# Optimization experiments

Hardware: AMD Instinct MI355X
Metric: run time of the kernel (lower is better)

## Reference

```python
import jax, jax.numpy as jnp
import numpy as np

B, N, EMB, FEAT = 4, 32, 512, 512
DO = N * (N - 1) // 2  # do_num = 0.5*N*(N-1)


def _encoder(h, adj, Wt, a_src, a_dst):
    # GATencoderlayer (inferred): single-head GAT attention restricted to the
    # strictly-lower triangle so that I_A = I - attn is unit lower-triangular
    # (invertible) and causal_graph = I - I_A = attn is a nonneg. strict-lower DAG.
    feat = h @ Wt  # [B,N,F]
    scores = jax.nn.leaky_relu((feat @ a_src)[:, :, None] + (feat @ a_dst)[:, None, :], 0.2)
    strict_lower = jnp.tril(jnp.ones((N, N), dtype=bool), -1)
    mask = (adj > 0) & strict_lower
    attn = jax.nn.softmax(jnp.where(mask, scores, -1e9), axis=-1)
    attn = jnp.where(mask.any(-1, keepdims=True), attn, 0.0) * mask  # row 0 has no parents
    fU = jax.nn.relu(attn @ feat)  # [B,N,F]
    I_A = jnp.eye(N, dtype=h.dtype) - attn
    return fU, I_A[:, None]  # I_A: [B,1,N,N] (multihead=1)


def _decoder(h, W, Wt):
    # GATdecoderlayer (inferred): aggregate linearly-transformed features with the
    # provided (sampled) mixing matrix W.
    feat = h @ Wt  # [B',N,F]
    return jax.nn.relu(jnp.einsum('bij,bjf->bif', W[:, 0], feat))


def _computing(cg, eps_do, few, feb, fsw, fsb):
    # Vectorized form of the triple-nested do-calculus loops.
    # cg: [B,N,N] strictly-lower causal graph.
    Bc = cg.shape[0]
    a, b = np.triu_indices(N, 1)  # raw_do pairs, same (i<j) row-major order as the loops
    idx = np.arange(N)
    ja = idx[None, :] == a[:, None]  # [DO,N]
    jb = idx[None, :] == b[:, None]
    lower = np.tril(np.ones((N, N), dtype=bool), -1)  # j < i (loop range j<=i, i==j handled by eye)
    pos = cg > 0  # [B,N,N]
    P = (pos & jnp.asarray(lower)).astype(cg.dtype)  # parent sets pa(i) = {k<i: cg[i,k]>0}
    common = jnp.einsum('bik,bjk->bij', P, P) > 0    # pa(i) \cap pa(j) nonempty
    ja_ = ja[:, None, :]; jb_ = jb[:, None, :]       # j-axis one-hots [DO,1,N]
    ia_ = ja[:, :, None]; ib_ = jb[:, :, None]       # i-axis one-hots [DO,N,1]
    c23 = jnp.asarray(lower[None] & ((ja_ & ~ib_) | (jb_ & ~ia_)))          # [DO,N,N]
    c4 = jnp.asarray(lower[None] & ~ja_ & ~jb_ & ~ia_ & ~ib_)               # [DO,N,N]
    eye = jnp.eye(N, dtype=bool)
    label = eye[None, None] | (c23[None] & pos[:, None]) | (c4[None] & common[:, None])  # [B,DO,N,N]
    # intervened graph: zero rows a and b
    keep = jnp.asarray(~(ja | jb)).astype(cg.dtype)  # [DO,N]
    cgd = (cg[:, None] * keep[None, :, :, None]).reshape(Bc * DO, N, N) + jnp.eye(N, dtype=cg.dtype)
    I_A = jnp.linalg.inv(cgd)[:, None]  # [B*DO,1,N,N]
    e = few[0, 0] * I_A + feb[0]  # Linear(1,1) applied elementwise
    s = fsw[0, 0] * I_A + fsb[0]
    z = e + jnp.exp(0.5 * s) * eps_do  # VAE reparameterization
    W_do = jnp.where(I_A == 0, I_A, z)
    return label.reshape(Bc * DO, N, N).astype(cg.dtype), W_do


def _forward(doc_sents_h, adj, enc_Wt, enc_asrc, enc_adst, dec_Wt, fce_w, fce_b, fcs_w, fcs_b, eps_main, eps_do):
    fU, I_A = _encoder(doc_sents_h, adj, enc_Wt, enc_asrc, enc_adst)
    causal_graph = jnp.eye(N, dtype=doc_sents_h.dtype) - I_A  # [B,1,N,N]
    inv = jnp.linalg.inv(I_A)
    e = fce_w[0, 0] * inv + fce_b[0]
    s = fcs_w[0, 0] * inv + fcs_b[0]
    z = e + jnp.exp(0.5 * s) * eps_main
    W = jnp.where(inv == 0, inv, z)
    X_raw = _decoder(fU, W, dec_Wt)
    label, W_do = _computing(causal_graph[:, 0], eps_do, fce_w, fce_b, fcs_w, fcs_b)
    h_do = jnp.broadcast_to(fU[:, None], (B, DO, N, FEAT)).reshape(B * DO, N, FEAT)
    X_do = _decoder(h_do, W_do, dec_Wt)
    return X_raw, X_do, label, causal_graph, e, s


def setup_inputs():
    key = jax.random.key(0)
    ks = jax.random.split(key, 10)
    return {
        'doc_sents_h': jax.random.normal(ks[0], (B, N, EMB), jnp.float32) * 0.5,
        'adj': jnp.ones((B, N, N), jnp.float32),
        'doc_len': jnp.full((B,), N, jnp.int32),
        'enc_Wt': jax.random.normal(ks[1], (EMB, FEAT), jnp.float32) / np.sqrt(EMB).astype(np.float32),
        'enc_asrc': jax.random.normal(ks[2], (FEAT,), jnp.float32) * 0.1,
        'enc_adst': jax.random.normal(ks[3], (FEAT,), jnp.float32) * 0.1,
        'dec_Wt': jax.random.normal(ks[4], (FEAT, FEAT), jnp.float32) / np.sqrt(FEAT).astype(np.float32),
        'fce_w': jax.random.normal(ks[5], (1, 1), jnp.float32) * 0.1,
        'fce_b': jax.random.normal(ks[6], (1,), jnp.float32) * 0.1,
        'fcs_w': jax.random.normal(ks[7], (1, 1), jnp.float32) * 0.1,
        'fcs_b': jax.random.normal(ks[8], (1,), jnp.float32) * 0.1,
        'eps_main': jax.random.normal(ks[9], (B, 1, N, N), jnp.float32),
        'eps_do': jax.random.normal(jax.random.fold_in(key, 1), (B * DO, 1, N, N), jnp.float32),
    }


def reference(doc_sents_h, adj, doc_len, enc_Wt, enc_asrc, enc_adst, dec_Wt, fce_w, fce_b, fcs_w, fcs_b, eps_main, eps_do):
    del doc_len  # original only asserts max(doc_len) == max_doc_len
    return _forward(doc_sents_h, adj, enc_Wt, enc_asrc, enc_adst, dec_Wt, fce_w, fce_b, fcs_w, fcs_b, eps_main, eps_do)
```

## Files before the change

kernel.cpp:

```cpp
#include <hip/hip_runtime.h>
#include <math.h>

#define N 32
#define B 4
#define EMB 512
#define FEAT 512
#define NDO 496
#define BDO (B*NDO)

#define OFF_XRAW  ((size_t)0)
#define OFF_XDO   ((size_t)(B*N*FEAT))
#define OFF_LABEL (OFF_XDO + (size_t)BDO*N*FEAT)
#define OFF_CG    (OFF_LABEL + (size_t)BDO*N*N)
#define OFF_E     (OFF_CG + (size_t)B*N*N)
#define OFF_S     (OFF_E + (size_t)B*N*N)

#define WS_FEAT   0
#define WS_ATTN   (WS_FEAT + B*N*FEAT)
#define WS_W      (WS_ATTN + B*N*N)
#define WS_FU     (WS_W + B*N*N)
#define WS_FEAT2  (WS_FU + B*N*FEAT)
#define WS_POS    (WS_FEAT2 + B*N*FEAT)
#define WS_COM    (WS_POS + B*N)

__global__ __launch_bounds__(128) void rowgemm4_kernel(
    const float* __restrict__ X, const float* __restrict__ Wt,
    float* __restrict__ out)
{
    __shared__ __align__(16) float ht[512][4];
    __shared__ __align__(16) float red[64 * 4];
    const int rg  = blockIdx.x >> 3;
    const int ch  = blockIdx.x & 7;
    const int tid = threadIdx.x;
    const int c   = tid & 63;
    const int kh  = tid >> 6;
    for (int idx = tid; idx < 2048; idx += 128) {
        const int r = idx >> 9, k = idx & 511;
        ht[k][r] = X[(size_t)(rg * 4 + r) * 512 + k];
    }
    __syncthreads();
    float a0 = 0.f, a1 = 0.f, a2 = 0.f, a3 = 0.f;
    const float* wp = Wt + (size_t)(kh * 256) * 512 + ch * 64 + c;
    const float4* hp = reinterpret_cast<const float4*>(&ht[kh * 256][0]);
    #pragma unroll 8
    for (int k = 0; k < 256; ++k) {
        const float w = wp[(size_t)k * 512];
        const float4 h4 = hp[k];
        a0 = fmaf(w, h4.x, a0); a1 = fmaf(w, h4.y, a1);
        a2 = fmaf(w, h4.z, a2); a3 = fmaf(w, h4.w, a3);
    }
    if (kh) *reinterpret_cast<float4*>(&red[c * 4]) = make_float4(a0, a1, a2, a3);
    __syncthreads();
    if (!kh) {
        const float4 r4 = *reinterpret_cast<const float4*>(&red[c * 4]);
        const size_t base = (size_t)(rg * 4) * 512 + ch * 64 + c;
        out[base]            = a0 + r4.x;
        out[base + 512]      = a1 + r4.y;
        out[base + 1024]     = a2 + r4.z;
        out[base + 1536]     = a3 + r4.w;
    }
}

__global__ __launch_bounds__(256) void batch_kernel(
    const float* __restrict__ adj, const float* __restrict__ featp,
    const float* __restrict__ a_src, const float* __restrict__ a_dst,
    const float* __restrict__ fce_w, const float* __restrict__ fce_b,
    const float* __restrict__ fcs_w, const float* __restrict__ fcs_b,
    const float* __restrict__ eps_main,
    float* __restrict__ out,
    float* __restrict__ ws_attn, float* __restrict__ ws_W,
    float* __restrict__ ws_fU,
    unsigned* __restrict__ posb, unsigned* __restrict__ comb)
{
    __shared__ float attnL[N * N];
    __shared__ float Minv[N * N];
    __shared__ float srcS[N], dstS[N];
    __shared__ unsigned pbits[N];
    const int b = blockIdx.x;
    const int tid = threadIdx.x;
    {
        const int row = tid >> 3, seg = tid & 7;
        const float* fp = featp + (size_t)(b * N + row) * 512 + seg * 64;
        const float* as = a_src + seg * 64;
        const float* ad = a_dst + seg * 64;
        float ps = 0.f, pd = 0.f;
        #pragma unroll
        for (int q = 0; q < 16; ++q) {
            const float4 f  = reinterpret_cast<const float4*>(fp)[q];
            const float4 s4 = reinterpret_cast<const float4*>(as)[q];
            const float4 d4 = reinterpret_cast<const float4*>(ad)[q];
            ps += f.x * s4.x + f.y * s4.y + f.z * s4.z + f.w * s4.w;
            pd += f.x * d4.x + f.y * d4.y + f.z * d4.z + f.w * d4.w;
        }
        ps += __shfl_down(ps, 4); pd += __shfl_down(pd, 4);
        ps += __shfl_down(ps, 2); pd += __shfl_down(pd, 2);
        ps += __shfl_down(ps, 1); pd += __shfl_down(pd, 1);
        if ((tid & 7) == 0) { srcS[row] = ps; dstS[row] = pd; }
    }
    __syncthreads();
    if (tid < N) {
        const int i = tid;
        const float srcv = srcS[i];
        const float* arow = adj + (size_t)b * N * N + i * N;
        float sc[N];
        float mx = -3e38f;
        bool any = false;
        #pragma unroll
        for (int j = 0; j < N; ++j) {
            const bool m = (arow[j] > 0.f) && (j < i);
            float x = srcv + dstS[j];
            x = (x >= 0.f) ? x : 0.2f * x;
            sc[j] = m ? x : -3e38f;
            if (m) { any = true; mx = fmaxf(mx, x); }
        }
        float den = 0.f;
        #pragma unroll
        for (int j = 0; j < N; ++j) {
            const float e = (sc[j] > -1e38f) ? __expf(sc[j] - mx) : 0.f;
            sc[j] = e;
            den += e;
        }
        const float inv_den = any ? (1.f / den) : 0.f;
        unsigned pb = 0;
        #pragma unroll
        for (int j = 0; j < N; ++j) {
            const float a = sc[j] * inv_den;
            attnL[i * N + j] = a;
            if (a > 0.f) pb |= (1u << j);
        }
        pbits[i] = pb;
        posb[b * N + i] = pb;
    }
    __syncthreads();
    for (int idx = tid; idx < N * N; idx += 256) {
        const float a = attnL[idx];
        out[OFF_CG + (size_t)b * N * N + idx] = a;
        ws_attn[b * N * N + idx] = a;
    }
    if (tid < N) {
        const unsigned my = pbits[tid];
        unsigned cb = 0;
        #pragma unroll
        for (int j = 0; j < N; ++j) if (my & pbits[j]) cb |= (1u << j);
        comb[b * N + tid] = cb;
    }
    if (tid < N) {
        const int j = tid;
        float x[N];
        #pragma unroll
        for (int i = 0; i < N; ++i) {
            float s = (i == j) ? 1.f : 0.f;
            #pragma unroll
            for (int k = 0; k < N; ++k)
                if (k < i) s = fmaf(attnL[i * N + k], x[k], s);
            x[i] = s;
            Minv[i * N + j] = s;
        }
    }
    __syncthreads();
    const float few = fce_w[0], feb = fce_b[0], fsw = fcs_w[0], fsb = fcs_b[0];
    for (int idx = tid; idx < N * N; idx += 256) {
        const float m = Minv[idx];
        const float e = fmaf(few, m, feb);
        const float s2 = fmaf(fsw, m, fsb);
        out[OFF_E + (size_t)b * N * N + idx] = e;
        out[OFF_S + (size_t)b * N * N + idx] = s2;
        ws_W[b * N * N + idx] = (m == 0.f) ? 0.f
            : fmaf(__expf(0.5f * s2), eps_main[b * N * N + idx], e);
    }
    const int c = 2 * tid;
    float2 v[N];
    #pragma unroll
    for (int j = 0; j < N; ++j)
        v[j] = *reinterpret_cast<const float2*>(&featp[(size_t)(b * N + j) * FEAT + c]);
    #pragma unroll
    for (int i = 0; i < N; ++i) {
        float s0 = 0.f, s1 = 0.f;
        #pragma unroll
        for (int j4 = 0; j4 < 8; ++j4) {
            if (4 * j4 < i) {
                const float4 w = *reinterpret_cast<const float4*>(&attnL[i * N + 4 * j4]);
                s0 = fmaf(w.x, v[4*j4+0].x, s0); s1 = fmaf(w.x, v[4*j4+0].y, s1);
                s0 = fmaf(w.y, v[4*j4+1].x, s0); s1 = fmaf(w.y, v[4*j4+1].y, s1);
                s0 = fmaf(w.z, v[4*j4+2].x, s0); s1 = fmaf(w.z, v[4*j4+2].y, s1);
                s0 = fmaf(w.w, v[4*j4+3].x, s0); s1 = fmaf(w.w, v[4*j4+3].y, s1);
            }
        }
        *reinterpret_cast<float2*>(&ws_fU[(size_t)(b * N + i) * FEAT + c]) =
            make_float2(fmaxf(s0, 0.f), fmaxf(s1, 0.f));
    }
}

__global__ __launch_bounds__(128) void xraw_kernel(
    const float* __restrict__ ws_W, const float* __restrict__ ws_feat2,
    float* __restrict__ out)
{
    const int row = blockIdx.x;
    const int b = row >> 5, i = row & 31;
    __shared__ float Wrow[N];
    const int tid = threadIdx.x;
    if (tid < N) Wrow[tid] = ws_W[(size_t)b * N * N + i * N + tid];
    __syncthreads();
    const int c = 4 * tid;
    float4 acc = make_float4(0.f, 0.f, 0.f, 0.f);
    #pragma unroll
    for (int j = 0; j < N; ++j) {
        const float w = Wrow[j];
        const float4 f = *reinterpret_cast<const float4*>(&ws_feat2[(size_t)(b * N + j) * FEAT + c]);
        acc.x = fmaf(w, f.x, acc.x); acc.y = fmaf(w, f.y, acc.y);
        acc.z = fmaf(w, f.z, acc.z); acc.w = fmaf(w, f.w, acc.w);
    }
    *reinterpret_cast<float4*>(&out[OFF_XRAW + (size_t)row * FEAT + c]) =
        make_float4(fmaxf(acc.x, 0.f), fmaxf(acc.y, 0.f), fmaxf(acc.z, 0.f), fmaxf(acc.w, 0.f));
}

__global__ __launch_bounds__(256) void do_kernel(
    const float* __restrict__ ws_attn, const float* __restrict__ ws_feat2,
    const unsigned* __restrict__ posb, const unsigned* __restrict__ comb,
    const float* __restrict__ fce_w, const float* __restrict__ fce_b,
    const float* __restrict__ fcs_w, const float* __restrict__ fcs_b,
    const float* __restrict__ eps_do,
    float* __restrict__ out)
{
    __shared__ float L[N * N];
    __shared__ float Minv[N * N];
    __shared__ float Wd[N * N];
    const int p = blockIdx.x;
    const int b = p / NDO;
    int tt = p - b * NDO;
    int ai = 0, rem = N - 1;
    while (tt >= rem) { tt -= rem; ++ai; --rem; }
    const int bi = ai + 1 + tt;
    const int tid = threadIdx.x;
    const int i0 = tid >> 3;
    const int j0 = (tid & 7) * 4;
    float4 lv = *reinterpret_cast<const float4*>(&ws_attn[(size_t)b * N * N + 4 * tid]);
    if (i0 == ai || i0 == bi) lv = make_float4(0.f, 0.f, 0.f, 0.f);
    *reinterpret_cast<float4*>(&L[4 * tid]) = lv;
    const float4 ev = *reinterpret_cast<const float4*>(&eps_do[(size_t)p * N * N + 4 * tid]);
    {
        const unsigned pb = posb[b * N + i0];
        const unsigned cb = comb[b * N + i0];
        float4 lab;
        float* lp = &lab.x;
        #pragma unroll
        for (int q = 0; q < 4; ++q) {
            const int j = j0 + q;
            const bool lower = i0 > j;
            const bool c23 = lower && (((j == ai) && (i0 != bi)) || ((j == bi) && (i0 != ai)));
            const bool c4 = lower && (i0 != ai) && (i0 != bi) && (j != ai) && (j != bi);
            const bool pos = (pb >> j) & 1u;
            const bool com = (cb >> j) & 1u;
            lp[q] = ((i0 == j) || (c23 && pos) || (c4 && com)) ? 1.f : 0.f;
        }
        *reinterpret_cast<float4*>(&out[OFF_LABEL + (size_t)p * N * N + 4 * tid]) = lab;
    }
    float v0[N];
    #pragma unroll
    for (int j = 0; j < N; ++j)
        v0[j] = ws_feat2[(size_t)(b * N + j) * FEAT + tid];
    __syncthreads();
    if (tid < N) {
        const int j = tid;
        float x[N];
        #pragma unroll
        for (int i = 0; i < N; ++i) {
            float s = (i == j) ? 1.f : 0.f;
            #pragma unroll
            for (int k = 0; k < N; ++k)
                if (k < i) s = fmaf(-L[i * N + k], x[k], s);
            x[i] = s;
            Minv[i * N + j] = s;
        }
    }
    __syncthreads();
    const float few = fce_w[0], feb = fce_b[0], fsw = fcs_w[0], fsb = fcs_b[0];
    {
        const float4 m4 = *reinterpret_cast<const float4*>(&Minv[4 * tid]);
        const float* mp = &m4.x;
        const float* ep = &ev.x;
        float4 w4;
        float* wp = &w4.x;
        #pragma unroll
        for (int q = 0; q < 4; ++q) {
            const float m = mp[q];
            const float e = fmaf(few, m, feb);
            const float s2 = fmaf(fsw, m, fsb);
            wp[q] = (m == 0.f) ? 0.f : fmaf(__expf(0.5f * s2), ep[q], e);
        }
        *reinterpret_cast<float4*>(&Wd[4 * tid]) = w4;
    }
    __syncthreads();
    float* Xdo = out + OFF_XDO + (size_t)p * N * FEAT;
    float v1[N];
    #pragma unroll
    for (int j = 0; j < N; ++j)
        v1[j] = ws_feat2[(size_t)(b * N + j) * FEAT + 256 + tid];
    #pragma unroll
    for (int i = 0; i < N; ++i) {
        float s = 0.f;
        #pragma unroll
        for (int j4 = 0; j4 < 8; ++j4) {
            if (4 * j4 <= i) {
                const float4 w = *reinterpret_cast<const float4*>(&Wd[i * N + 4 * j4]);
                s = fmaf(w.x, v0[4*j4+0], s);
                s = fmaf(w.y, v0[4*j4+1], s);
                s = fmaf(w.z, v0[4*j4+2], s);
                s = fmaf(w.w, v0[4*j4+3], s);
            }
        }
        Xdo[(size_t)i * FEAT + tid] = fmaxf(s, 0.f);
    }
    #pragma unroll
    for (int i = 0; i < N; ++i) {
        float s = 0.f;
        #pragma unroll
        for (int j4 = 0; j4 < 8; ++j4) {
            if (4 * j4 <= i) {
                const float4 w = *reinterpret_cast<const float4*>(&Wd[i * N + 4 * j4]);
                s = fmaf(w.x, v1[4*j4+0], s);
                s = fmaf(w.y, v1[4*j4+1], s);
                s = fmaf(w.z, v1[4*j4+2], s);
                s = fmaf(w.w, v1[4*j4+3], s);
            }
        }
        Xdo[(size_t)i * FEAT + 256 + tid] = fmaxf(s, 0.f);
    }
}

extern "C" void kernel_launch(void* const* d_in, const int* in_sizes, int n_in,
                              void* d_out, int out_size, void* d_ws, size_t ws_size,
                              hipStream_t stream)
{
    const float* h        = (const float*)d_in[0];
    const float* adj      = (const float*)d_in[1];
    const float* enc_Wt   = (const float*)d_in[3];
    const float* a_src    = (const float*)d_in[4];
    const float* a_dst    = (const float*)d_in[5];
    const float* dec_Wt   = (const float*)d_in[6];
    const float* fce_w    = (const float*)d_in[7];
    const float* fce_b    = (const float*)d_in[8];
    const float* fcs_w    = (const float*)d_in[9];
    const float* fcs_b    = (const float*)d_in[10];
    const float* eps_main = (const float*)d_in[11];
    const float* eps_do   = (const float*)d_in[12];
    float* out = (float*)d_out;
    float* ws  = (float*)d_ws;

    float* ws_feat  = ws + WS_FEAT;
    float* ws_attn  = ws + WS_ATTN;
    float* ws_W     = ws + WS_W;
    float* ws_fU    = ws + WS_FU;
    float* ws_feat2 = ws + WS_FEAT2;
    unsigned* ws_pos = (unsigned*)(ws + WS_POS);
    unsigned* ws_com = (unsigned*)(ws + WS_COM);

    rowgemm4_kernel<<<256, 128, 0, stream>>>(h, enc_Wt, ws_feat);
    batch_kernel<<<B, 256, 0, stream>>>(
        adj, ws_feat, a_src, a_dst, fce_w, fce_b, fcs_w, fcs_b,
        eps_main, out, ws_attn, ws_W, ws_fU, ws_pos, ws_com);
    rowgemm4_kernel<<<256, 128, 0, stream>>>(ws_fU, dec_Wt, ws_feat2);
    xraw_kernel<<<B * N, 128, 0, stream>>>(ws_W, ws_feat2, out);
    do_kernel<<<BDO, 256, 0, stream>>>(
        ws_attn, ws_feat2, ws_pos, ws_com, fce_w, fce_b, fcs_w, fcs_b,
        eps_do, out);
}
```

Before: 113.6 us.

## Split do_kernel into triangular-inverse kernel and half-width Xdo GEMM kernel

The fused do_kernel becomes two kernels. A 64-thread invert_kernel computes the per-intervention inverse, the sampled W and the labels, and stores W to workspace, or into the Xdo output region when workspace is too small. A separate xdo_kernel then runs twice as many blocks, each handling half the feature columns, so the serial 32-thread inversion no longer idles a 256-thread block and more waves are available for the bandwidth-bound output writes. In exchange it adds a launch and a global round-trip for W, and drops the triangular skip in the inner product.

```diff
diff --git a/kernel.cpp b/kernel.cpp
--- a/kernel.cpp
+++ b/kernel.cpp
@@ -22,6 +22,7 @@
 #define WS_FEAT2  (WS_FU + B*N*FEAT)
 #define WS_POS    (WS_FEAT2 + B*N*FEAT)
 #define WS_COM    (WS_POS + B*N)
+#define WS_WD     (WS_COM + B*N)
 
 __global__ __launch_bounds__(128) void rowgemm4_kernel(
     const float* __restrict__ X, const float* __restrict__ Wt,
@@ -214,117 +215,117 @@
         make_float4(fmaxf(acc.x, 0.f), fmaxf(acc.y, 0.f), fmaxf(acc.z, 0.f), fmaxf(acc.w, 0.f));
 }
 
-__global__ __launch_bounds__(256) void do_kernel(
-    const float* __restrict__ ws_attn, const float* __restrict__ ws_feat2,
+__global__ __launch_bounds__(64) void invert_kernel(
+    const float* __restrict__ ws_attn,
     const unsigned* __restrict__ posb, const unsigned* __restrict__ comb,
     const float* __restrict__ fce_w, const float* __restrict__ fce_b,
     const float* __restrict__ fcs_w, const float* __restrict__ fcs_b,
     const float* __restrict__ eps_do,
+    float* __restrict__ wd_buf, size_t wd_stride,
     float* __restrict__ out)
 {
-    __shared__ float L[N * N];
+    __shared__ float A[N * N];
     __shared__ float Minv[N * N];
-    __shared__ float Wd[N * N];
     const int p = blockIdx.x;
     const int b = p / NDO;
     int tt = p - b * NDO;
     int ai = 0, rem = N - 1;
     while (tt >= rem) { tt -= rem; ++ai; --rem; }
     const int bi = ai + 1 + tt;
-    const int tid = threadIdx.x;
-    const int i0 = tid >> 3;
-    const int j0 = (tid & 7) * 4;
-    float4 lv = *reinterpret_cast<const float4*>(&ws_attn[(size_t)b * N * N + 4 * tid]);
-    if (i0 == ai || i0 == bi) lv = make_float4(0.f, 0.f, 0.f, 0.f);
-    *reinterpret_cast<float4*>(&L[4 * tid]) = lv;
-    const float4 ev = *reinterpret_cast<const float4*>(&eps_do[(size_t)p * N * N + 4 * tid]);
-    {
-        const unsigned pb = posb[b * N + i0];
-        const unsigned cb = comb[b * N + i0];
-        float4 lab;
-        float* lp = &lab.x;
-        #pragma unroll
-        for (int q = 0; q < 4; ++q) {
-            const int j = j0 + q;
-            const bool lower = i0 > j;
-            const bool c23 = lower && (((j == ai) && (i0 != bi)) || ((j == bi) && (i0 != ai)));
-            const bool c4 = lower && (i0 != ai) && (i0 != bi) && (j != ai) && (j != bi);
-            const bool pos = (pb >> j) & 1u;
-            const bool com = (cb >> j) & 1u;
-            lp[q] = ((i0 == j) || (c23 && pos) || (c4 && com)) ? 1.f : 0.f;
-        }
-        *reinterpret_cast<float4*>(&out[OFF_LABEL + (size_t)p * N * N + 4 * tid]) = lab;
-    }
-    float v0[N];
-    #pragma unroll
-    for (int j = 0; j < N; ++j)
-        v0[j] = ws_feat2[(size_t)(b * N + j) * FEAT + tid];
-    __syncthreads();
-    if (tid < N) {
-        const int j = tid;
+    const int lane = threadIdx.x;
+    #pragma unroll
+    for (int q = 0; q < 4; ++q) {
+        const int base = q * 256 + 4 * lane;
+        *reinterpret_cast<float4*>(&A[base]) =
+            *reinterpret_cast<const float4*>(&ws_attn[(size_t)b * N * N + base]);
+    }
+    __syncthreads();
+    if (lane < N) {
+        const int j = lane;
         float x[N];
         #pragma unroll
         for (int i = 0; i < N; ++i) {
-            float s = (i == j) ? 1.f : 0.f;
-            #pragma unroll
-            for (int k = 0; k < N; ++k)
-                if (k < i) s = fmaf(-L[i * N + k], x[k], s);
-            x[i] = s;
-            Minv[i * N + j] = s;
+            if (i == ai || i == bi) {
+                x[i] = (i == j) ? 1.f : 0.f;
+            } else {
+                float s = (i == j) ? 1.f : 0.f;
+                #pragma unroll
+                for (int k = 0; k < N; ++k)
+                    if (k < i) s = fmaf(-A[i * N + k], x[k], s);
+                x[i] = s;
+            }
+            Minv[i * N + j] = x[i];
         }
     }
     __syncthreads();
     const float few = fce_w[0], feb = fce_b[0], fsw = fcs_w[0], fsb = fcs_b[0];
-    {
-        const float4 m4 = *reinterpret_cast<const float4*>(&Minv[4 * tid]);
+    #pragma unroll
+    for (int q = 0; q < 4; ++q) {
+        const int base = q * 256 + 4 * lane;
+        const int i = base >> 5, j0 = base & 31;
+        const float4 m4 = *reinterpret_cast<const float4*>(&Minv[base]);
+        const float4 e4 = *reinterpret_cast<const float4*>(&eps_do[(size_t)p * N * N + base]);
         const float* mp = &m4.x;
-        const float* ep = &ev.x;
-        float4 w4;
+        const float* ep = &e4.x;
+        float4 w4, lab4;
         float* wp = &w4.x;
-        #pragma unroll
-        for (int q = 0; q < 4; ++q) {
-            const float m = mp[q];
+        float* lp = &lab4.x;
+        const unsigned pb = posb[b * N + i];
+        const unsigned cb = comb[b * N + i];
+        #pragma unroll
+        for (int q2 = 0; q2 < 4; ++q2) {
+            const float m = mp[q2];
             const float e = fmaf(few, m, feb);
             const float s2 = fmaf(fsw, m, fsb);
-            wp[q] = (m == 0.f) ? 0.f : fmaf(__expf(0.5f * s2), ep[q], e);
-        }
-        *reinterpret_cast<float4*>(&Wd[4 * tid]) = w4;
-    }
+            wp[q2] = (m == 0.f) ? 0.f : fmaf(__expf(0.5f * s2), ep[q2], e);
+            const int j = j0 + q2;
+            const bool lower = i > j;
+            const bool c23 = lower && (((j == ai) && (i != bi)) || ((j == bi) && (i != ai)));
+            const bool c4 = lower && (i != ai) && (i != bi) && (j != ai) && (j != bi);
+            lp[q2] = ((i == j) || (c23 && ((pb >> j) & 1u)) || (c4 && ((cb >> j) & 1u)))
+                         ? 1.f : 0.f;
+        }
+        *reinterpret_cast<float4*>(&wd_buf[(size_t)p * wd_stride + base]) = w4;
+        *reinterpret_cast<float4*>(&out[OFF_LABEL + (size_t)p * N * N + base]) = lab4;
+    }
+}
+
+__global__ __launch_bounds__(256) void xdo_kernel(
+    const float* __restrict__ wd_buf, size_t wd_stride,
+    const float* __restrict__ ws_feat2,
+    float* __restrict__ out)
+{
+    __shared__ __align__(16) float Wd[N * N];
+    const int blk = blockIdx.x;
+    const int p = blk >> 1;
+    const int half = blk & 1;
+    const int b = p / NDO;
+    const int tid = threadIdx.x;
+    *reinterpret_cast<float4*>(&Wd[4 * tid]) =
+        *reinterpret_cast<const float4*>(&wd_buf[(size_t)p * wd_stride + 4 * tid]);
+    const int col = half * 256 + tid;
+    float v[N];
+    #pragma unroll
+    for (int k = 0; k < N; ++k)
+        v[k] = ws_feat2[(size_t)(b * N + k) * FEAT + col];
     __syncthreads();
     float* Xdo = out + OFF_XDO + (size_t)p * N * FEAT;
-    float v1[N];
-    #pragma unroll
-    for (int j = 0; j < N; ++j)
-        v1[j] = ws_feat2[(size_t)(b * N + j) * FEAT + 256 + tid];
-    #pragma unroll
+    #pragma unroll 2
     for (int i = 0; i < N; ++i) {
-        float s = 0.f;
-        #pragma unroll
-        for (int j4 = 0; j4 < 8; ++j4) {
-            if (4 * j4 <= i) {
-                const float4 w = *reinterpret_cast<const float4*>(&Wd[i * N + 4 * j4]);
-                s = fmaf(w.x, v0[4*j4+0], s);
-                s = fmaf(w.y, v0[4*j4+1], s);
-                s = fmaf(w.z, v0[4*j4+2], s);
-                s = fmaf(w.w, v0[4*j4+3], s);
-            }
-        }
-        Xdo[(size_t)i * FEAT + tid] = fmaxf(s, 0.f);
-    }
-    #pragma unroll
-    for (int i = 0; i < N; ++i) {
-        float s = 0.f;
-        #pragma unroll
-        for (int j4 = 0; j4 < 8; ++j4) {
-            if (4 * j4 <= i) {
-                const float4 w = *reinterpret_cast<const float4*>(&Wd[i * N + 4 * j4]);
-                s = fmaf(w.x, v1[4*j4+0], s);
-                s = fmaf(w.y, v1[4*j4+1], s);
-                s = fmaf(w.z, v1[4*j4+2], s);
-                s = fmaf(w.w, v1[4*j4+3], s);
-            }
-        }
-        Xdo[(size_t)i * FEAT + 256 + tid] = fmaxf(s, 0.f);
+        float s0 = 0.f, s1 = 0.f;
+        #pragma unroll
+        for (int u = 0; u < 4; ++u) {
+            const float4 w = *reinterpret_cast<const float4*>(&Wd[i * N + 4 * u]);
+            s0 = fmaf(w.x, v[4*u+0], s0); s0 = fmaf(w.y, v[4*u+1], s0);
+            s0 = fmaf(w.z, v[4*u+2], s0); s0 = fmaf(w.w, v[4*u+3], s0);
+        }
+        #pragma unroll
+        for (int u = 4; u < 8; ++u) {
+            const float4 w = *reinterpret_cast<const float4*>(&Wd[i * N + 4 * u]);
+            s1 = fmaf(w.x, v[4*u+0], s1); s1 = fmaf(w.y, v[4*u+1], s1);
+            s1 = fmaf(w.z, v[4*u+2], s1); s1 = fmaf(w.w, v[4*u+3], s1);
+        }
+        Xdo[(size_t)i * FEAT + col] = fmaxf(s0 + s1, 0.f);
     }
 }
 
@@ -355,13 +356,20 @@
     unsigned* ws_pos = (unsigned*)(ws + WS_POS);
     unsigned* ws_com = (unsigned*)(ws + WS_COM);
 
+    const size_t need = (size_t)(WS_WD + BDO * N * N) * sizeof(float);
+    float* wd_buf;
+    size_t wd_stride;
+    if (ws_size >= need) { wd_buf = ws + WS_WD;       wd_stride = N * N; }
+    else                 { wd_buf = out + OFF_XDO;    wd_stride = N * FEAT; }
+
     rowgemm4_kernel<<<256, 128, 0, stream>>>(h, enc_Wt, ws_feat);
     batch_kernel<<<B, 256, 0, stream>>>(
         adj, ws_feat, a_src, a_dst, fce_w, fce_b, fcs_w, fcs_b,
         eps_main, out, ws_attn, ws_W, ws_fU, ws_pos, ws_com);
     rowgemm4_kernel<<<256, 128, 0, stream>>>(ws_fU, dec_Wt, ws_feat2);
     xraw_kernel<<<B * N, 128, 0, stream>>>(ws_W, ws_feat2, out);
-    do_kernel<<<BDO, 256, 0, stream>>>(
-        ws_attn, ws_feat2, ws_pos, ws_com, fce_w, fce_b, fcs_w, fcs_b,
-        eps_do, out);
-}
+    invert_kernel<<<BDO, 64, 0, stream>>>(
+        ws_attn, ws_pos, ws_com, fce_w, fce_b, fcs_w, fcs_b,
+        eps_do, wd_buf, wd_stride, out);
+    xdo_kernel<<<2 * BDO, 256, 0, stream>>>(wd_buf, wd_stride, ws_feat2, out);
+}
```

Measured after the change: 111.4 us. No clear change (-1.9%).
